# Kernel tuning notes

Measured on AMD Instinct MI355X. Metric: run time of the kernel, lower is better.

The kernel has to match this reference:

```python
import jax, jax.numpy as jnp
import numpy as np

B = 16
SR = 16000
DUR = 3
L = SR * DUR          # 48000 samples
W = 64                # n_wavetables
LWT = 512             # wavetable_len


def setup_inputs() -> dict:
    key = jax.random.key(0)
    k1, k2, k3, k4 = jax.random.split(key, 4)
    # Per-sample F0 in a realistic range (CREPE-style, upsampled to sr)
    pitch = jax.random.uniform(k1, (B, L), dtype=jnp.float32, minval=50.0, maxval=500.0)
    envelope = jax.random.uniform(k2, (B, L, 1), dtype=jnp.float32)
    # attention is "already softmaxed" per the docstring
    attention = jax.nn.softmax(jax.random.normal(k3, (B, L, W), dtype=jnp.float32), axis=-1)
    # Wavetable bank: first 4 are fixed sines with cycles 1..4, rest N(0, 0.01)
    i = jnp.arange(LWT, dtype=jnp.float32)
    fixed = jnp.stack([jnp.sin(c * 2.0 * jnp.pi * i / LWT) for c in (1, 2, 3, 4)], axis=0)
    learned = 0.01 * jax.random.normal(k4, (W - 4, LWT), dtype=jnp.float32)
    wavetables = jnp.concatenate([fixed, learned], axis=0)  # [W, LWT]
    return {"pitch": pitch, "envelope": envelope, "attention": attention, "wavetables": wavetables}


def reference(pitch, envelope, attention, wavetables):
    lwt = wavetables.shape[1]
    # phase increment per sample, per batch item: [B, L]
    increment = (lwt / SR) * pitch
    # NOTE: faithful to original torch code: subtracts the FIRST BATCH ROW
    # of increments (broadcast over batch), not a per-row first element.
    index = jnp.cumsum(increment, axis=1) - increment[0]
    index = jnp.remainder(index, lwt)
    index = jnp.where(lwt - index < 1e-05, 0.0, index)
    low = jnp.floor(index)
    alpha = index - low                       # [B, L]
    idx_low = low.astype(jnp.int32)           # in [0, lwt-1]
    idx_high = jnp.ceil(index).astype(jnp.int32) % lwt
    # Dual gather across all 64 wavetables at once: [W, B, L]
    wl = wavetables[:, idx_low]
    wh = wavetables[:, idx_high]
    waves = wl + alpha[None, :, :] * (wh - wl)  # linear interpolation
    # attention-weighted sum over wavetables, then envelope: [B, L, 1]
    out = jnp.einsum('wbl,blw->bl', waves, attention)[..., None] * envelope
    return out
```

## Files before the change

kernel.cpp:

```cpp
#include <hip/hip_runtime.h>
#include <hip/hip_fp16.h>

#define BB    16
#define LL    48000
#define WW    64
#define LWT   512
#define CHUNK 750
#define NCH   64
#define NELEM (BB*LL)
#define NGRP  (NELEM/4)
#define RATIO (512.0/16000.0)

__global__ void kT(const float* __restrict__ wt, __half* __restrict__ tab) {
    int tid = blockIdx.x * 256 + threadIdx.x;
    int idx = tid >> 6, w = tid & 63;
    tab[tid] = __float2half(wt[w * LWT + idx]);
}

__global__ void kA(const float* __restrict__ pitch, double* __restrict__ csum) {
    int bid = blockIdx.x;
    int r = bid >> 6, c = bid & 63;
    int t = threadIdx.x;
    double s = 0.0;
    if (t < 250) {
        const float* p = pitch + r * LL + c * CHUNK + t * 3;
        s = RATIO * (double)p[0] + RATIO * (double)p[1] + RATIO * (double)p[2];
    }
    for (int d = 1; d < 64; d <<= 1) s += __shfl_xor(s, d);
    __shared__ double wsh[4];
    if ((t & 63) == 0) wsh[t >> 6] = s;
    __syncthreads();
    if (t == 0) csum[bid] = wsh[0] + wsh[1] + wsh[2] + wsh[3];
}

__global__ void kB(const double* __restrict__ csum, double* __restrict__ cbase) {
    int r = threadIdx.x >> 6, c = threadIdx.x & 63;
    double v = csum[r * NCH + c];
    double inc = v;
    for (int d = 1; d < 64; d <<= 1) {
        double u = __shfl_up(inc, d);
        if (c >= d) inc += u;
    }
    cbase[r * NCH + c] = inc - v;
}

__global__ void kC(const float* __restrict__ pitch,
                   const double* __restrict__ cbase,
                   unsigned* __restrict__ packed) {
    int bid = blockIdx.x;
    int r = bid >> 6, c = bid & 63;
    int t = threadIdx.x;
    int lane = t & 63, wv = t >> 6;
    int l = c * CHUNK + t * 3;
    bool act = (t < 250);
    double i0 = 0.0, i1 = 0.0, i2 = 0.0;
    if (act) {
        const float* p = pitch + r * LL + l;
        i0 = RATIO * (double)p[0];
        i1 = RATIO * (double)p[1];
        i2 = RATIO * (double)p[2];
    }
    double c0 = i0, c1 = i0 + i1, c2 = c1 + i2;
    double inc = c2;
    for (int d = 1; d < 64; d <<= 1) {
        double u = __shfl_up(inc, d);
        if (lane >= d) inc += u;
    }
    __shared__ double wsum[4];
    if (lane == 63) wsum[wv] = inc;
    __syncthreads();
    double wb = 0.0;
    for (int i = 0; i < wv; i++) wb += wsum[i];
    if (!act) return;
    double base = cbase[bid] + (wb + inc - c2);
    double pre[3] = {c0, c1, c2};
    for (int k = 0; k < 3; k++) {
        double inc0 = RATIO * (double)pitch[l + k];
        double idx = base + pre[k] - inc0;
        double m = idx - floor(idx * (1.0 / 512.0)) * 512.0;
        if (m < 0.0) m += 512.0;
        if (512.0 - m < 1e-5) m = 0.0;
        double lowd = floor(m);
        double alpha = m - lowd;
        unsigned il = (unsigned)lowd;
        unsigned au = (unsigned)(alpha * 8388608.0 + 0.5);
        if (au > 0x7fffffu) au = 0x7fffffu;
        packed[r * LL + l + k] = (il << 23) | au;
    }
}

__global__ __launch_bounds__(256) void kD(const float4* __restrict__ attn4,
                                          const float* __restrict__ env,
                                          const unsigned* __restrict__ packed,
                                          const __half* __restrict__ tabG,
                                          float* __restrict__ out) {
    __shared__ __half tab[LWT * WW];
    {
        const uint4* s4 = (const uint4*)tabG;
        uint4* d4 = (uint4*)tab;
        for (int i = threadIdx.x; i < (LWT * WW) / 8; i += 256) d4[i] = s4[i];
    }
    __syncthreads();
    const int lane = threadIdx.x & 63;
    const int sub = lane >> 4;
    const int li  = lane & 15;
    const int wid = (blockIdx.x << 2) | (threadIdx.x >> 6);
    const int gpw = 94;
    int g0 = wid * gpw;
    int g1 = g0 + gpw;
    if (g1 > NGRP) g1 = NGRP;
    if (g0 >= g1) return;

    float4  a = attn4[(size_t)g0 * 64 + lane];
    unsigned p = packed[(g0 << 2) | sub];
    for (int g = g0; g < g1; ++g) {
        float4 ac = a;
        unsigned pc = p;
        int gn = g + 1;
        if (gn < g1) {
            a = attn4[(size_t)gn * 64 + lane];
            p = packed[(gn << 2) | sub];
        }
        unsigned il = pc >> 23;
        float alpha = (float)(pc & 0x7fffffu) * (1.0f / 8388608.0f);
        unsigned ih = (il + 1) & 511;
        uint2 lo = *(const uint2*)(tab + (il << 6) + (li << 2));
        uint2 hi = *(const uint2*)(tab + (ih << 6) + (li << 2));
        __half2 l01 = *(__half2*)&lo.x, l23 = *(__half2*)&lo.y;
        __half2 h01 = *(__half2*)&hi.x, h23 = *(__half2*)&hi.y;
        float2 fl01 = __half22float2(l01), fl23 = __half22float2(l23);
        float2 fh01 = __half22float2(h01), fh23 = __half22float2(h23);
        float w0 = fmaf(alpha, fh01.x - fl01.x, fl01.x);
        float w1 = fmaf(alpha, fh01.y - fl01.y, fl01.y);
        float w2 = fmaf(alpha, fh23.x - fl23.x, fl23.x);
        float w3 = fmaf(alpha, fh23.y - fl23.y, fl23.y);
        float s = w0 * ac.x + w1 * ac.y + w2 * ac.z + w3 * ac.w;
        s += __shfl_xor(s, 1);
        s += __shfl_xor(s, 2);
        s += __shfl_xor(s, 4);
        s += __shfl_xor(s, 8);
        if (li == 0) {
            int e = (g << 2) | sub;
            out[e] = s * env[e];
        }
    }
}

extern "C" void kernel_launch(void* const* d_in, const int* in_sizes, int n_in,
                              void* d_out, int out_size, void* d_ws, size_t ws_size,
                              hipStream_t stream) {
    const float* pitch = (const float*)d_in[0];
    const float* env   = (const float*)d_in[1];
    const float* attn  = (const float*)d_in[2];
    const float* wt    = (const float*)d_in[3];
    float* out = (float*)d_out;

    char* ws = (char*)d_ws;
    __half*   tab    = (__half*)(ws);
    double*   csum   = (double*)(ws + 65536);
    double*   cbase  = (double*)(ws + 73728);
    unsigned* packed = (unsigned*)(ws + 81920);

    kT<<<128, 256, 0, stream>>>(wt, tab);
    kA<<<BB * NCH, 256, 0, stream>>>(pitch, csum);
    kB<<<1, 1024, 0, stream>>>(csum, cbase);
    kC<<<BB * NCH, 256, 0, stream>>>(pitch, cbase, packed);
    kD<<<512, 256, 0, stream>>>((const float4*)attn, env, packed, tab, out);
}
```

Baseline: 321.8 us.

## Merge table transpose into scan kernel, double kD threads, prefetch two groups ahead

The wavetable transpose kernel is folded into kA as extra blocks, which removes one launch. kD now runs 512 threads per block, doubling the waves that share each 64KB shared-memory table copy, so per-wave work shrinks. The attention/packed prefetch is deepened from one group ahead to two to keep more memory requests in flight. The cost is more registers per thread and a larger block, which can limit occupancy.

```diff
diff --git a/kernel.cpp b/kernel.cpp
--- a/kernel.cpp
+++ b/kernel.cpp
@@ -11,14 +11,20 @@
 #define NGRP  (NELEM/4)
 #define RATIO (512.0/16000.0)
 
-__global__ void kT(const float* __restrict__ wt, __half* __restrict__ tab) {
-    int tid = blockIdx.x * 256 + threadIdx.x;
-    int idx = tid >> 6, w = tid & 63;
-    tab[tid] = __float2half(wt[w * LWT + idx]);
-}
+#define KD_THREADS 512
+#define KD_BLOCKS  512
+#define KD_WAVES   (KD_BLOCKS * (KD_THREADS/64))
+#define GPW        ((NGRP + KD_WAVES - 1) / KD_WAVES)
 
-__global__ void kA(const float* __restrict__ pitch, double* __restrict__ csum) {
+__global__ void kA(const float* __restrict__ pitch, double* __restrict__ csum,
+                   const float* __restrict__ wt, __half* __restrict__ tab) {
     int bid = blockIdx.x;
+    if (bid >= BB * NCH) {
+        int tid = (bid - BB * NCH) * 256 + threadIdx.x;
+        int idx = tid >> 6, w = tid & 63;
+        tab[tid] = __float2half(wt[w * LWT + idx]);
+        return;
+    }
     int r = bid >> 6, c = bid & 63;
     int t = threadIdx.x;
     double s = 0.0;
@@ -89,37 +95,43 @@
     }
 }
 
-__global__ __launch_bounds__(256) void kD(const float4* __restrict__ attn4,
-                                          const float* __restrict__ env,
-                                          const unsigned* __restrict__ packed,
-                                          const __half* __restrict__ tabG,
-                                          float* __restrict__ out) {
+__global__ __launch_bounds__(KD_THREADS) void kD(const float4* __restrict__ attn4,
+                                                 const float* __restrict__ env,
+                                                 const unsigned* __restrict__ packed,
+                                                 const __half* __restrict__ tabG,
+                                                 float* __restrict__ out) {
     __shared__ __half tab[LWT * WW];
     {
         const uint4* s4 = (const uint4*)tabG;
         uint4* d4 = (uint4*)tab;
-        for (int i = threadIdx.x; i < (LWT * WW) / 8; i += 256) d4[i] = s4[i];
+        for (int i = threadIdx.x; i < (LWT * WW) / 8; i += KD_THREADS) d4[i] = s4[i];
     }
     __syncthreads();
     const int lane = threadIdx.x & 63;
     const int sub = lane >> 4;
     const int li  = lane & 15;
-    const int wid = (blockIdx.x << 2) | (threadIdx.x >> 6);
-    const int gpw = 94;
-    int g0 = wid * gpw;
-    int g1 = g0 + gpw;
+    const int wid = (blockIdx.x << 3) | (threadIdx.x >> 6);
+    int g0 = wid * GPW;
+    int g1 = g0 + GPW;
     if (g1 > NGRP) g1 = NGRP;
     if (g0 >= g1) return;
 
-    float4  a = attn4[(size_t)g0 * 64 + lane];
-    unsigned p = packed[(g0 << 2) | sub];
+    float4  a0 = attn4[(size_t)g0 * 64 + lane];
+    unsigned p0 = packed[(g0 << 2) | sub];
+    float4  a1 = a0;
+    unsigned p1 = p0;
+    if (g0 + 1 < g1) {
+        a1 = attn4[(size_t)(g0 + 1) * 64 + lane];
+        p1 = packed[((g0 + 1) << 2) | sub];
+    }
     for (int g = g0; g < g1; ++g) {
-        float4 ac = a;
-        unsigned pc = p;
-        int gn = g + 1;
+        float4 ac = a0;
+        unsigned pc = p0;
+        a0 = a1; p0 = p1;
+        int gn = g + 2;
         if (gn < g1) {
-            a = attn4[(size_t)gn * 64 + lane];
-            p = packed[(gn << 2) | sub];
+            a1 = attn4[(size_t)gn * 64 + lane];
+            p1 = packed[(gn << 2) | sub];
         }
         unsigned il = pc >> 23;
         float alpha = (float)(pc & 0x7fffffu) * (1.0f / 8388608.0f);
@@ -161,9 +173,8 @@
     double*   cbase  = (double*)(ws + 73728);
     unsigned* packed = (unsigned*)(ws + 81920);
 
-    kT<<<128, 256, 0, stream>>>(wt, tab);
-    kA<<<BB * NCH, 256, 0, stream>>>(pitch, csum);
+    kA<<<BB * NCH + 128, 256, 0, stream>>>(pitch, csum, wt, tab);
     kB<<<1, 1024, 0, stream>>>(csum, cbase);
     kC<<<BB * NCH, 256, 0, stream>>>(pitch, cbase, packed);
-    kD<<<512, 256, 0, stream>>>((const float4*)attn, env, packed, tab, out);
+    kD<<<KD_BLOCKS, KD_THREADS, 0, stream>>>((const float4*)attn, env, packed, tab, out);
 }
```

Measured after the change: 292.4 us. 1.1x faster.
